# Performance work log

Measured on AMD Instinct MI355X. Metric: run time of the kernel, lower is better.

Reference implementation:

```python
import jax, jax.numpy as jnp
import numpy as np

D = 1024  # in_features
H = 16    # head_num

def setup_inputs() -> dict:
    key = jax.random.key(0)
    ks = jax.random.split(key, 11)
    S, B = 2048, 2
    scale = 1.0 / np.sqrt(D)
    inp = {
        'q': jax.random.normal(ks[0], (S, B, D), jnp.float32),
        'k': jax.random.normal(ks[1], (S, B, D), jnp.float32),
        'v': jax.random.normal(ks[2], (S, B, D), jnp.float32),
        'Wq': jax.random.normal(ks[3], (D, D), jnp.float32) * scale,
        'Wk': jax.random.normal(ks[4], (D, D), jnp.float32) * scale,
        'Wv': jax.random.normal(ks[5], (D, D), jnp.float32) * scale,
        'Wo': jax.random.normal(ks[6], (D, D), jnp.float32) * scale,
        'bq': jax.random.normal(ks[7], (D,), jnp.float32) * 0.01,
        'bk': jax.random.normal(ks[8], (D,), jnp.float32) * 0.01,
        'bv': jax.random.normal(ks[9], (D,), jnp.float32) * 0.01,
        'bo': jax.random.normal(ks[10], (D,), jnp.float32) * 0.01,
    }
    return inp

def reference(q, k, v, Wq, Wk, Wv, Wo, bq, bk, bv, bo):
    # q,k,v: (S, B, D) -> (B, S, D)
    q = jnp.transpose(q, (1, 0, 2))
    k = jnp.transpose(k, (1, 0, 2))
    v = jnp.transpose(v, (1, 0, 2))
    # linear + ReLU (torch Linear: x @ W.T + b)
    qh = jax.nn.relu(q @ Wq.T + bq)
    kh = jax.nn.relu(k @ Wk.T + bk)
    vh = jax.nn.relu(v @ Wv.T + bv)
    B, S, _ = qh.shape
    hd = D // H
    # (B, S, H, hd) -> (B, H, S, hd)
    qh = qh.reshape(B, S, H, hd).transpose(0, 2, 1, 3)
    kh = kh.reshape(B, S, H, hd).transpose(0, 2, 1, 3)
    vh = vh.reshape(B, S, H, hd).transpose(0, 2, 1, 3)
    scores = jnp.einsum('bhsd,bhtd->bhst', qh, kh) / np.sqrt(hd).astype(np.float32)
    attn = jax.nn.softmax(scores, axis=-1)
    y = jnp.einsum('bhst,bhtd->bhsd', attn, vh)  # (B, H, S, hd)
    y = y.transpose(0, 2, 1, 3).reshape(B, S, D)
    y = jax.nn.relu(y @ Wo.T + bo)
    return jnp.transpose(y, (1, 0, 2))  # (S, B, D)
```

## Files before the change

### kernel.cpp

```cpp
#include <hip/hip_runtime.h>
#include <stdint.h>

typedef __attribute__((ext_vector_type(8))) short bf8v;
typedef __attribute__((ext_vector_type(4))) float f4v;
typedef __attribute__((ext_vector_type(16))) float f16v;
typedef __attribute__((ext_vector_type(4))) unsigned int u4v;

__device__ __forceinline__ unsigned short f2bf(float f) {
  unsigned int u = __float_as_uint(f);
  u += 0x7fffu + ((u >> 16) & 1u);
  return (unsigned short)(u >> 16);
}

__device__ __forceinline__ void gload16(const void* g, void* l) {
  __builtin_amdgcn_global_load_lds(
      (__attribute__((address_space(1))) void*)reinterpret_cast<uintptr_t>(g),
      (__attribute__((address_space(3))) void*)reinterpret_cast<uintptr_t>(l),
      16, 0, 0);
}

__device__ __forceinline__ unsigned cvtpk(float lo, float hi) {
  unsigned r;
  asm("v_cvt_pk_bf16_f32 %0, %1, %2" : "=v"(r) : "v"(lo), "v"(hi));
  return r;
}

__global__ __launch_bounds__(256) void cvt_many(
    const float* __restrict__ s0, const float* __restrict__ s1,
    const float* __restrict__ s2, const float* __restrict__ s3,
    unsigned short* __restrict__ d0, unsigned short* __restrict__ d1,
    unsigned short* __restrict__ d2, unsigned short* __restrict__ d3, int n) {
  int a = blockIdx.y;
  const float* src = (a == 0) ? s0 : (a == 1) ? s1 : (a == 2) ? s2 : s3;
  unsigned short* dst = (a == 0) ? d0 : (a == 1) ? d1 : (a == 2) ? d2 : d3;
  int i = (blockIdx.x * 256 + threadIdx.x) * 8;
  if (i >= n) return;
  const f4v* sp = (const f4v*)(src + i);
  f4v x = sp[0], y = sp[1];
  bf8v r;
  r[0] = (short)f2bf(x[0]); r[1] = (short)f2bf(x[1]);
  r[2] = (short)f2bf(x[2]); r[3] = (short)f2bf(x[3]);
  r[4] = (short)f2bf(y[0]); r[5] = (short)f2bf(y[1]);
  r[6] = (short)f2bf(y[2]); r[7] = (short)f2bf(y[3]);
  *(bf8v*)(dst + i) = r;
}

template <int OMODE>
__device__ __forceinline__ void gemm_body(
    unsigned short* Al, unsigned short* Bl,
    const unsigned short* __restrict__ A, const unsigned short* __restrict__ W,
    const float* __restrict__ bias, void* __restrict__ out) {
  const int tid = threadIdx.x;
  const int w = tid >> 6, l = tid & 63;
  const int lr = l >> 4, lc = l & 15;
  const int m0 = blockIdx.x * 128, n0 = blockIdx.y * 128;
  const int wr = w >> 1, wc = w & 1;

  f4v acc[4][4];
#pragma unroll
  for (int i = 0; i < 4; i++)
#pragma unroll
    for (int j = 0; j < 4; j++) acc[i][j] = (f4v)(0.0f);

  const int NK = 32;
#pragma unroll
  for (int i = 0; i < 2; i++) {
    int chunk = w * 2 + i;
    int e = (chunk * 1024 + l * 16) >> 1;
    int r = e >> 5, k = e & 31;
    gload16(A + (size_t)(m0 + r) * 1024 + k, Al + chunk * 512);
    gload16(W + (size_t)(n0 + r) * 1024 + k, Bl + chunk * 512);
  }

  for (int kk = 0; kk < NK; kk++) {
    const int cur = kk & 1;
    __syncthreads();
    if (kk + 1 < NK) {
#pragma unroll
      for (int i = 0; i < 2; i++) {
        int chunk = w * 2 + i;
        int e = (chunk * 1024 + l * 16) >> 1;
        int r = e >> 5, k = (kk + 1) * 32 + (e & 31);
        gload16(A + (size_t)(m0 + r) * 1024 + k, Al + (cur ^ 1) * 4096 + chunk * 512);
        gload16(W + (size_t)(n0 + r) * 1024 + k, Bl + (cur ^ 1) * 4096 + chunk * 512);
      }
    }
    bf8v av[4], bv[4];
#pragma unroll
    for (int i = 0; i < 4; i++) {
      int row = wr * 64 + i * 16 + lc;
      av[i] = *(const bf8v*)(Al + cur * 4096 + row * 32 + lr * 8);
    }
#pragma unroll
    for (int j = 0; j < 4; j++) {
      int row = wc * 64 + j * 16 + lc;
      bv[j] = *(const bf8v*)(Bl + cur * 4096 + row * 32 + lr * 8);
    }
#pragma unroll
    for (int i = 0; i < 4; i++)
#pragma unroll
      for (int j = 0; j < 4; j++)
        acc[i][j] = __builtin_amdgcn_mfma_f32_16x16x32_bf16(av[i], bv[j], acc[i][j], 0, 0, 0);
  }

#pragma unroll
  for (int j = 0; j < 4; j++) {
    int n = n0 + wc * 64 + j * 16 + lc;
    float bj = bias[n];
#pragma unroll
    for (int i = 0; i < 4; i++) {
      int mb = m0 + wr * 64 + i * 16 + lr * 4;
#pragma unroll
      for (int q = 0; q < 4; q++) {
        float val = fmaxf(acc[i][j][q] + bj, 0.0f);
        int m = mb + q;
        if (OMODE == 2) {
          int s = m & 2047, b = m >> 11;
          ((float*)out)[(size_t)(s * 2 + b) * 1024 + n] = val;
        } else {
          int s = m >> 1, b = m & 1;
          int h = n >> 6, d = n & 63;
          if (OMODE == 0)
            ((unsigned short*)out)[((size_t)(b * 16 + h) * 2048 + s) * 64 + d] = f2bf(val);
          else
            ((unsigned short*)out)[((size_t)(b * 16 + h) * 64 + d) * 2048 + s] = f2bf(val);
        }
      }
    }
  }
}

__global__ __launch_bounds__(256) void qkv_gemm(
    const unsigned short* __restrict__ qA, const unsigned short* __restrict__ kA,
    const unsigned short* __restrict__ vA,
    const unsigned short* __restrict__ Wq, const unsigned short* __restrict__ Wk,
    const unsigned short* __restrict__ Wv,
    const float* __restrict__ bq, const float* __restrict__ bk,
    const float* __restrict__ bv,
    unsigned short* __restrict__ Qh, unsigned short* __restrict__ Kh,
    unsigned short* __restrict__ Vt) {
  __shared__ __align__(16) unsigned short Al[2 * 4096];
  __shared__ __align__(16) unsigned short Bl[2 * 4096];
  int z = blockIdx.z;
  if (z == 0)      gemm_body<0>(Al, Bl, qA, Wq, bq, Qh);
  else if (z == 1) gemm_body<0>(Al, Bl, kA, Wk, bk, Kh);
  else             gemm_body<1>(Al, Bl, vA, Wv, bv, Vt);
}

__global__ __launch_bounds__(256) void out_gemm(
    const unsigned short* __restrict__ Y, const unsigned short* __restrict__ Wo,
    const float* __restrict__ bo, float* __restrict__ out) {
  __shared__ __align__(16) unsigned short Al[2 * 4096];
  __shared__ __align__(16) unsigned short Bl[2 * 4096];
  gemm_body<2>(Al, Bl, Y, Wo, bo, out);
}

__global__ __launch_bounds__(128, 1) void attn_kernel(
    const unsigned short* __restrict__ Qh, const unsigned short* __restrict__ Kh,
    const unsigned short* __restrict__ Vt, unsigned short* __restrict__ Y) {
  __shared__ __align__(16) unsigned short Kl[2][4096];
  __shared__ __align__(16) unsigned short Vl[2][4096];
  const int tid = threadIdx.x, w = tid >> 6, l = tid & 63;
  const int lo = l & 31, hi = l >> 5;
  const int bh = blockIdx.y;
  const int q0 = blockIdx.x * 128 + w * 64;
  const size_t qkbase = (size_t)bh * 2048 * 64;
  const size_t vtbase = (size_t)bh * 64 * 2048;
  const float cs = 0.125f * 1.44269504088896341f;

  bf8v qf[2][4];
#pragma unroll
  for (int s = 0; s < 2; s++)
#pragma unroll
    for (int c = 0; c < 4; c++)
      qf[s][c] = *(const bf8v*)(Qh + qkbase + (size_t)(q0 + s * 32 + lo) * 64 + c * 16 + hi * 8);

  f16v oacc[2][2];
#pragma unroll
  for (int s = 0; s < 2; s++)
#pragma unroll
    for (int dt = 0; dt < 2; dt++) oacc[s][dt] = (f16v)(0.0f);
  float mrun[2] = {-1e30f, -1e30f}, lrun[2] = {0.0f, 0.0f};

  const int swl = (lo & 7) << 4;
  int akb[4], avb[2][2][2];
#pragma unroll
  for (int c = 0; c < 4; c++) akb[c] = lo * 128 + ((c * 32 + hi * 16) ^ swl);
#pragma unroll
  for (int dt = 0; dt < 2; dt++)
#pragma unroll
    for (int kvh = 0; kvh < 2; kvh++)
#pragma unroll
      for (int kc = 0; kc < 2; kc++)
        avb[dt][kvh][kc] = (dt * 32 + lo) * 128 + ((kvh * 64 + kc * 32 + hi * 16) ^ swl);

  int stE[4], stD[4], stKV[4];
#pragma unroll
  for (int i = 0; i < 4; i++) {
    int o = (w * 4 + i) * 1024 + l * 16;
    int row = o >> 7;
    stE[i] = (o ^ ((row & 7) << 4)) >> 1;
    stD[i] = stE[i] >> 6;
    stKV[i] = stE[i] & 63;
  }
  const char* KlB = (const char*)&Kl[0][0];
  const char* VlB = (const char*)&Vl[0][0];

  auto STAGE = [&](int buf, int t0) {
#pragma unroll
    for (int i = 0; i < 4; i++) {
      gload16(Kh + qkbase + (size_t)t0 * 64 + stE[i], (char*)&Kl[buf][0] + (w * 4 + i) * 1024);
      gload16(Vt + vtbase + (size_t)stD[i] * 2048 + t0 + stKV[i], (char*)&Vl[buf][0] + (w * 4 + i) * 1024);
    }
  };

  auto COMPUTE = [&](int bo) {
#pragma unroll
    for (int kvh = 0; kvh < 2; kvh++) {
      bf8v kf[4];
#pragma unroll
      for (int c = 0; c < 4; c++)
        kf[c] = *(const bf8v*)(KlB + bo + kvh * 4096 + akb[c]);
      f16v sa = (f16v)(0.0f), sb = (f16v)(0.0f);
#pragma unroll
      for (int c = 0; c < 4; c++) {
        sa = __builtin_amdgcn_mfma_f32_32x32x16_bf16(kf[c], qf[0][c], sa, 0, 0, 0);
        sb = __builtin_amdgcn_mfma_f32_32x32x16_bf16(kf[c], qf[1][c], sb, 0, 0, 0);
      }
      bf8v vf[2][2];
#pragma unroll
      for (int dt = 0; dt < 2; dt++)
#pragma unroll
        for (int kc = 0; kc < 2; kc++)
          vf[dt][kc] = *(const bf8v*)(VlB + bo + avb[dt][kvh][kc]);

#pragma unroll
      for (int s = 0; s < 2; s++) {
        const f16v& sc16 = (s == 0) ? sa : sb;
        float m16 = sc16[0];
#pragma unroll
        for (int r = 1; r < 16; r++) m16 = fmaxf(m16, sc16[r]);
        m16 = fmaxf(m16, __shfl_xor(m16, 32));
        float msc = m16 * cs;
        if (!__all(msc <= mrun[s] + 8.0f)) {
          float mnew = fmaxf(mrun[s], msc);
          float scl = __builtin_amdgcn_exp2f(mrun[s] - mnew);
          lrun[s] *= scl;
#pragma unroll
          for (int dt = 0; dt < 2; dt++)
#pragma unroll
            for (int r = 0; r < 16; r++) oacc[s][dt][r] *= scl;
          mrun[s] = mnew;
        }
        float p[16];
        float rs = 0.0f;
#pragma unroll
        for (int r = 0; r < 16; r++) {
          p[r] = __builtin_amdgcn_exp2f(sc16[r] * cs - mrun[s]);
          rs += p[r];
        }
        rs += __shfl_xor(rs, 32);
        lrun[s] += rs;
        bf8v pf[2];
#pragma unroll
        for (int kc = 0; kc < 2; kc++) {
          unsigned a0 = cvtpk(p[kc * 8 + 0], p[kc * 8 + 1]);
          unsigned a1 = cvtpk(p[kc * 8 + 2], p[kc * 8 + 3]);
          unsigned b0 = cvtpk(p[kc * 8 + 4], p[kc * 8 + 5]);
          unsigned b1 = cvtpk(p[kc * 8 + 6], p[kc * 8 + 7]);
          asm("v_permlane32_swap_b32 %0, %1" : "+v"(a0), "+v"(b0));
          asm("v_permlane32_swap_b32 %0, %1" : "+v"(a1), "+v"(b1));
          u4v pw;
          pw[0] = a0; pw[1] = a1; pw[2] = b0; pw[3] = b1;
          pf[kc] = __builtin_bit_cast(bf8v, pw);
        }
#pragma unroll
        for (int dt = 0; dt < 2; dt++)
#pragma unroll
          for (int kc = 0; kc < 2; kc++)
            oacc[s][dt] = __builtin_amdgcn_mfma_f32_32x32x16_bf16(vf[dt][kc], pf[kc], oacc[s][dt], 0, 0, 0);
      }
    }
  };

  STAGE(0, 0);
  __syncthreads();
#pragma unroll 1
  for (int t0 = 0; t0 < 2048; t0 += 128) {
    STAGE(1, t0 + 64);
    COMPUTE(0);
    __syncthreads();
    if (t0 + 128 < 2048) STAGE(0, t0 + 128);
    COMPUTE(8192);
    __syncthreads();
  }

  const int b = bh >> 4, h = bh & 15;
#pragma unroll
  for (int s = 0; s < 2; s++) {
    float inv = 1.0f / lrun[s];
    int q = q0 + s * 32 + lo;
    size_t base = ((size_t)(b * 2048 + q) << 10) + h * 64;
#pragma unroll
    for (int dt = 0; dt < 2; dt++)
#pragma unroll
      for (int r = 0; r < 16; r++) {
        int d = dt * 32 + (r & 3) + 8 * (r >> 2) + 4 * hi;
        Y[base + d] = f2bf(oacc[s][dt][r] * inv);
      }
  }
}

extern "C" void kernel_launch(void* const* d_in, const int* in_sizes, int n_in,
                              void* d_out, int out_size, void* d_ws, size_t ws_size,
                              hipStream_t stream) {
  const float* q  = (const float*)d_in[0];
  const float* k  = (const float*)d_in[1];
  const float* v  = (const float*)d_in[2];
  const float* Wq = (const float*)d_in[3];
  const float* Wk = (const float*)d_in[4];
  const float* Wv = (const float*)d_in[5];
  const float* Wo = (const float*)d_in[6];
  const float* bq = (const float*)d_in[7];
  const float* bk = (const float*)d_in[8];
  const float* bv = (const float*)d_in[9];
  const float* bo = (const float*)d_in[10];

  const size_t NA = (size_t)4096 * 1024;
  const size_t NW = (size_t)1024 * 1024;
  unsigned short* qA  = (unsigned short*)d_ws;
  unsigned short* kA  = qA  + NA;
  unsigned short* vA  = kA  + NA;
  unsigned short* WqB = vA  + NA;
  unsigned short* WkB = WqB + NW;
  unsigned short* WvB = WkB + NW;
  unsigned short* WoB = WvB + NW;
  unsigned short* Qh  = WoB + NW;
  unsigned short* Kh  = Qh  + NA;
  unsigned short* Vt  = Kh  + NA;
  unsigned short* Y   = Vt  + NA;

  cvt_many<<<dim3(2048, 3), 256, 0, stream>>>(q, k, v, nullptr, qA, kA, vA, nullptr, (int)NA);
  cvt_many<<<dim3(512, 4), 256, 0, stream>>>(Wq, Wk, Wv, Wo, WqB, WkB, WvB, WoB, (int)NW);

  qkv_gemm<<<dim3(32, 8, 3), 256, 0, stream>>>(qA, kA, vA, WqB, WkB, WvB,
                                               bq, bk, bv, Qh, Kh, Vt);
  attn_kernel<<<dim3(16, 32), 128, 0, stream>>>(Qh, Kh, Vt, Y);
  out_gemm<<<dim3(32, 8), 256, 0, stream>>>(Y, WoB, bo, (float*)d_out);
}
```

Measured before the change: 137.3 us.

## Load K/V directly to registers in attention and merge conversion launches

The attention kernel drops its LDS double-buffered staging with global_load_lds and barriers. Each single-wave block now loads K and V fragments straight from global memory into registers, ping-ponging between two register sets with 32-key steps, and the grid doubles to 32x32 blocks of 64 threads. The two fp32-to-bf16 conversion launches become one flat launch over the contiguous workspace, and the max reduction is rebalanced into a tree. This removes LDS traffic, syncs and one launch, at the cost of K/V reuse across waves, uncoalesced strided V loads, and more register pressure.

```diff
diff --git a/kernel.cpp b/kernel.cpp
--- a/kernel.cpp
+++ b/kernel.cpp
@@ -25,17 +25,26 @@
   return r;
 }
 
-__global__ __launch_bounds__(256) void cvt_many(
+__global__ __launch_bounds__(256) void cvt_all(
     const float* __restrict__ s0, const float* __restrict__ s1,
     const float* __restrict__ s2, const float* __restrict__ s3,
-    unsigned short* __restrict__ d0, unsigned short* __restrict__ d1,
-    unsigned short* __restrict__ d2, unsigned short* __restrict__ d3, int n) {
-  int a = blockIdx.y;
-  const float* src = (a == 0) ? s0 : (a == 1) ? s1 : (a == 2) ? s2 : s3;
-  unsigned short* dst = (a == 0) ? d0 : (a == 1) ? d1 : (a == 2) ? d2 : d3;
-  int i = (blockIdx.x * 256 + threadIdx.x) * 8;
-  if (i >= n) return;
-  const f4v* sp = (const f4v*)(src + i);
+    const float* __restrict__ s4, const float* __restrict__ s5,
+    const float* __restrict__ s6, unsigned short* __restrict__ dst) {
+  const size_t NA = (size_t)1 << 22, NW = (size_t)1 << 20;
+  size_t i = ((size_t)blockIdx.x * 256 + threadIdx.x) * 8;
+  const float* src;
+  size_t off;
+  if (i < 3 * NA) {
+    int a = (int)(i >> 22);
+    src = (a == 0) ? s0 : (a == 1) ? s1 : s2;
+    off = i & (NA - 1);
+  } else {
+    size_t j = i - 3 * NA;
+    int a = (int)(j >> 20);
+    src = (a == 0) ? s3 : (a == 1) ? s4 : (a == 2) ? s5 : s6;
+    off = j & (NW - 1);
+  }
+  const f4v* sp = (const f4v*)(src + off);
   f4v x = sp[0], y = sp[1];
   bf8v r;
   r[0] = (short)f2bf(x[0]); r[1] = (short)f2bf(x[1]);
@@ -155,17 +164,15 @@
   gemm_body<2>(Al, Bl, Y, Wo, bo, out);
 }
 
-__global__ __launch_bounds__(128, 1) void attn_kernel(
+__global__ __launch_bounds__(64, 1) void attn_kernel(
     const unsigned short* __restrict__ Qh, const unsigned short* __restrict__ Kh,
     const unsigned short* __restrict__ Vt, unsigned short* __restrict__ Y) {
-  __shared__ __align__(16) unsigned short Kl[2][4096];
-  __shared__ __align__(16) unsigned short Vl[2][4096];
-  const int tid = threadIdx.x, w = tid >> 6, l = tid & 63;
+  const int l = threadIdx.x & 63;
   const int lo = l & 31, hi = l >> 5;
   const int bh = blockIdx.y;
-  const int q0 = blockIdx.x * 128 + w * 64;
-  const size_t qkbase = (size_t)bh * 2048 * 64;
-  const size_t vtbase = (size_t)bh * 64 * 2048;
+  const int q0 = blockIdx.x * 64;
+  const unsigned short* __restrict__ Kb = Kh + (size_t)bh * 2048 * 64;
+  const unsigned short* __restrict__ Vb = Vt + (size_t)bh * 64 * 2048;
   const float cs = 0.125f * 1.44269504088896341f;
 
   bf8v qf[2][4];
@@ -173,7 +180,8 @@
   for (int s = 0; s < 2; s++)
 #pragma unroll
     for (int c = 0; c < 4; c++)
-      qf[s][c] = *(const bf8v*)(Qh + qkbase + (size_t)(q0 + s * 32 + lo) * 64 + c * 16 + hi * 8);
+      qf[s][c] = *(const bf8v*)(Qh + (size_t)bh * 2048 * 64 +
+                                (size_t)(q0 + s * 32 + lo) * 64 + c * 16 + hi * 8);
 
   f16v oacc[2][2];
 #pragma unroll
@@ -182,117 +190,85 @@
     for (int dt = 0; dt < 2; dt++) oacc[s][dt] = (f16v)(0.0f);
   float mrun[2] = {-1e30f, -1e30f}, lrun[2] = {0.0f, 0.0f};
 
-  const int swl = (lo & 7) << 4;
-  int akb[4], avb[2][2][2];
-#pragma unroll
-  for (int c = 0; c < 4; c++) akb[c] = lo * 128 + ((c * 32 + hi * 16) ^ swl);
-#pragma unroll
-  for (int dt = 0; dt < 2; dt++)
-#pragma unroll
-    for (int kvh = 0; kvh < 2; kvh++)
+  auto LOADKV = [&](bf8v (&kf)[4], bf8v (&vf)[4], int t) {
+#pragma unroll
+    for (int c = 0; c < 4; c++)
+      kf[c] = *(const bf8v*)(Kb + (size_t)(t + lo) * 64 + c * 16 + hi * 8);
+#pragma unroll
+    for (int dt = 0; dt < 2; dt++)
 #pragma unroll
       for (int kc = 0; kc < 2; kc++)
-        avb[dt][kvh][kc] = (dt * 32 + lo) * 128 + ((kvh * 64 + kc * 32 + hi * 16) ^ swl);
-
-  int stE[4], stD[4], stKV[4];
-#pragma unroll
-  for (int i = 0; i < 4; i++) {
-    int o = (w * 4 + i) * 1024 + l * 16;
-    int row = o >> 7;
-    stE[i] = (o ^ ((row & 7) << 4)) >> 1;
-    stD[i] = stE[i] >> 6;
-    stKV[i] = stE[i] & 63;
-  }
-  const char* KlB = (const char*)&Kl[0][0];
-  const char* VlB = (const char*)&Vl[0][0];
-
-  auto STAGE = [&](int buf, int t0) {
-#pragma unroll
-    for (int i = 0; i < 4; i++) {
-      gload16(Kh + qkbase + (size_t)t0 * 64 + stE[i], (char*)&Kl[buf][0] + (w * 4 + i) * 1024);
-      gload16(Vt + vtbase + (size_t)stD[i] * 2048 + t0 + stKV[i], (char*)&Vl[buf][0] + (w * 4 + i) * 1024);
-    }
+        vf[dt * 2 + kc] = *(const bf8v*)(Vb + (size_t)(dt * 32 + lo) * 2048 +
+                                         t + kc * 16 + hi * 8);
   };
 
-  auto COMPUTE = [&](int bo) {
-#pragma unroll
-    for (int kvh = 0; kvh < 2; kvh++) {
-      bf8v kf[4];
-#pragma unroll
-      for (int c = 0; c < 4; c++)
-        kf[c] = *(const bf8v*)(KlB + bo + kvh * 4096 + akb[c]);
-      f16v sa = (f16v)(0.0f), sb = (f16v)(0.0f);
-#pragma unroll
-      for (int c = 0; c < 4; c++) {
-        sa = __builtin_amdgcn_mfma_f32_32x32x16_bf16(kf[c], qf[0][c], sa, 0, 0, 0);
-        sb = __builtin_amdgcn_mfma_f32_32x32x16_bf16(kf[c], qf[1][c], sb, 0, 0, 0);
-      }
-      bf8v vf[2][2];
+  auto COMPUTE = [&](const bf8v (&kf)[4], const bf8v (&vf)[4]) {
+    f16v sa = (f16v)(0.0f), sb = (f16v)(0.0f);
+#pragma unroll
+    for (int c = 0; c < 4; c++) {
+      sa = __builtin_amdgcn_mfma_f32_32x32x16_bf16(kf[c], qf[0][c], sa, 0, 0, 0);
+      sb = __builtin_amdgcn_mfma_f32_32x32x16_bf16(kf[c], qf[1][c], sb, 0, 0, 0);
+    }
+#pragma unroll
+    for (int s = 0; s < 2; s++) {
+      const f16v& sc16 = (s == 0) ? sa : sb;
+      float m0a = fmaxf(fmaxf(sc16[0], sc16[1]), sc16[2]);
+      float m0b = fmaxf(fmaxf(sc16[3], sc16[4]), sc16[5]);
+      float m0c = fmaxf(fmaxf(sc16[6], sc16[7]), sc16[8]);
+      float m0d = fmaxf(fmaxf(sc16[9], sc16[10]), sc16[11]);
+      float m0e = fmaxf(fmaxf(sc16[12], sc16[13]), sc16[14]);
+      float m16 = fmaxf(fmaxf(fmaxf(m0a, m0b), fmaxf(m0c, m0d)), fmaxf(m0e, sc16[15]));
+      m16 = fmaxf(m16, __shfl_xor(m16, 32));
+      float msc = m16 * cs;
+      if (!__all(msc <= mrun[s] + 8.0f)) {
+        float mnew = fmaxf(mrun[s], msc);
+        float scl = __builtin_amdgcn_exp2f(mrun[s] - mnew);
+        lrun[s] *= scl;
+#pragma unroll
+        for (int dt = 0; dt < 2; dt++)
+#pragma unroll
+          for (int r = 0; r < 16; r++) oacc[s][dt][r] *= scl;
+        mrun[s] = mnew;
+      }
+      float p[16];
+      float rs = 0.0f;
+#pragma unroll
+      for (int r = 0; r < 16; r++) {
+        p[r] = __builtin_amdgcn_exp2f(sc16[r] * cs - mrun[s]);
+        rs += p[r];
+      }
+      rs += __shfl_xor(rs, 32);
+      lrun[s] += rs;
+      bf8v pf[2];
+#pragma unroll
+      for (int kc = 0; kc < 2; kc++) {
+        unsigned a0 = cvtpk(p[kc * 8 + 0], p[kc * 8 + 1]);
+        unsigned a1 = cvtpk(p[kc * 8 + 2], p[kc * 8 + 3]);
+        unsigned b0 = cvtpk(p[kc * 8 + 4], p[kc * 8 + 5]);
+        unsigned b1 = cvtpk(p[kc * 8 + 6], p[kc * 8 + 7]);
+        asm("v_permlane32_swap_b32 %0, %1" : "+v"(a0), "+v"(b0));
+        asm("v_permlane32_swap_b32 %0, %1" : "+v"(a1), "+v"(b1));
+        u4v pw;
+        pw[0] = a0; pw[1] = a1; pw[2] = b0; pw[3] = b1;
+        pf[kc] = __builtin_bit_cast(bf8v, pw);
+      }
 #pragma unroll
       for (int dt = 0; dt < 2; dt++)
 #pragma unroll
         for (int kc = 0; kc < 2; kc++)
-          vf[dt][kc] = *(const bf8v*)(VlB + bo + avb[dt][kvh][kc]);
-
-#pragma unroll
-      for (int s = 0; s < 2; s++) {
-        const f16v& sc16 = (s == 0) ? sa : sb;
-        float m16 = sc16[0];
-#pragma unroll
-        for (int r = 1; r < 16; r++) m16 = fmaxf(m16, sc16[r]);
-        m16 = fmaxf(m16, __shfl_xor(m16, 32));
-        float msc = m16 * cs;
-        if (!__all(msc <= mrun[s] + 8.0f)) {
-          float mnew = fmaxf(mrun[s], msc);
-          float scl = __builtin_amdgcn_exp2f(mrun[s] - mnew);
-          lrun[s] *= scl;
-#pragma unroll
-          for (int dt = 0; dt < 2; dt++)
-#pragma unroll
-            for (int r = 0; r < 16; r++) oacc[s][dt][r] *= scl;
-          mrun[s] = mnew;
-        }
-        float p[16];
-        float rs = 0.0f;
-#pragma unroll
-        for (int r = 0; r < 16; r++) {
-          p[r] = __builtin_amdgcn_exp2f(sc16[r] * cs - mrun[s]);
-          rs += p[r];
-        }
-        rs += __shfl_xor(rs, 32);
-        lrun[s] += rs;
-        bf8v pf[2];
-#pragma unroll
-        for (int kc = 0; kc < 2; kc++) {
-          unsigned a0 = cvtpk(p[kc * 8 + 0], p[kc * 8 + 1]);
-          unsigned a1 = cvtpk(p[kc * 8 + 2], p[kc * 8 + 3]);
-          unsigned b0 = cvtpk(p[kc * 8 + 4], p[kc * 8 + 5]);
-          unsigned b1 = cvtpk(p[kc * 8 + 6], p[kc * 8 + 7]);
-          asm("v_permlane32_swap_b32 %0, %1" : "+v"(a0), "+v"(b0));
-          asm("v_permlane32_swap_b32 %0, %1" : "+v"(a1), "+v"(b1));
-          u4v pw;
-          pw[0] = a0; pw[1] = a1; pw[2] = b0; pw[3] = b1;
-          pf[kc] = __builtin_bit_cast(bf8v, pw);
-        }
-#pragma unroll
-        for (int dt = 0; dt < 2; dt++)
-#pragma unroll
-          for (int kc = 0; kc < 2; kc++)
-            oacc[s][dt] = __builtin_amdgcn_mfma_f32_32x32x16_bf16(vf[dt][kc], pf[kc], oacc[s][dt], 0, 0, 0);
-      }
+          oacc[s][dt] = __builtin_amdgcn_mfma_f32_32x32x16_bf16(vf[dt * 2 + kc], pf[kc],
+                                                               oacc[s][dt], 0, 0, 0);
     }
   };
 
-  STAGE(0, 0);
-  __syncthreads();
+  bf8v kA[4], vA[4], kB[4], vB[4];
+  LOADKV(kA, vA, 0);
 #pragma unroll 1
-  for (int t0 = 0; t0 < 2048; t0 += 128) {
-    STAGE(1, t0 + 64);
-    COMPUTE(0);
-    __syncthreads();
-    if (t0 + 128 < 2048) STAGE(0, t0 + 128);
-    COMPUTE(8192);
-    __syncthreads();
+  for (int t = 0; t < 2048; t += 64) {
+    LOADKV(kB, vB, t + 32);
+    COMPUTE(kA, vA);
+    if (t + 64 < 2048) LOADKV(kA, vA, t + 64);
+    COMPUTE(kB, vB);
   }
 
   const int b = bh >> 4, h = bh & 15;
@@ -340,11 +316,10 @@
   unsigned short* Vt  = Kh  + NA;
   unsigned short* Y   = Vt  + NA;
 
-  cvt_many<<<dim3(2048, 3), 256, 0, stream>>>(q, k, v, nullptr, qA, kA, vA, nullptr, (int)NA);
-  cvt_many<<<dim3(512, 4), 256, 0, stream>>>(Wq, Wk, Wv, Wo, WqB, WkB, WvB, WoB, (int)NW);
+  cvt_all<<<dim3(8192), 256, 0, stream>>>(q, k, v, Wq, Wk, Wv, Wo, qA);
 
   qkv_gemm<<<dim3(32, 8, 3), 256, 0, stream>>>(qA, kA, vA, WqB, WkB, WvB,
                                                bq, bk, bv, Qh, Kh, Vt);
-  attn_kernel<<<dim3(16, 32), 128, 0, stream>>>(Qh, Kh, Vt, Y);
+  attn_kernel<<<dim3(32, 32), 64, 0, stream>>>(Qh, Kh, Vt, Y);
   out_gemm<<<dim3(32, 8), 256, 0, stream>>>(Y, WoB, bo, (float*)d_out);
 }
```

New measurement: 168.9 us. +23.0%, slower.

## Split attention query rows across four waves and merge conversion launches

Applied to the files above, without the earlier changes.

The attention kernel now runs 256 threads per block. Each wave handles 32 query rows instead of 64, and K/V staging is split over four waves. The aim is to raise occupancy and latency hiding, at the cost of less K/V fragment reuse per LDS read. The two fp32-to-bf16 conversion launches are merged into one flat kernel that writes into a contiguous workspace, removing one launch.

```diff
diff --git a/kernel.cpp b/kernel.cpp
--- a/kernel.cpp
+++ b/kernel.cpp
@@ -25,17 +25,26 @@
   return r;
 }
 
-__global__ __launch_bounds__(256) void cvt_many(
+__global__ __launch_bounds__(256) void cvt_all(
     const float* __restrict__ s0, const float* __restrict__ s1,
     const float* __restrict__ s2, const float* __restrict__ s3,
-    unsigned short* __restrict__ d0, unsigned short* __restrict__ d1,
-    unsigned short* __restrict__ d2, unsigned short* __restrict__ d3, int n) {
-  int a = blockIdx.y;
-  const float* src = (a == 0) ? s0 : (a == 1) ? s1 : (a == 2) ? s2 : s3;
-  unsigned short* dst = (a == 0) ? d0 : (a == 1) ? d1 : (a == 2) ? d2 : d3;
-  int i = (blockIdx.x * 256 + threadIdx.x) * 8;
-  if (i >= n) return;
-  const f4v* sp = (const f4v*)(src + i);
+    const float* __restrict__ s4, const float* __restrict__ s5,
+    const float* __restrict__ s6, unsigned short* __restrict__ dst) {
+  const size_t NA = (size_t)1 << 22, NW = (size_t)1 << 20;
+  size_t i = ((size_t)blockIdx.x * 256 + threadIdx.x) * 8;
+  const float* src;
+  size_t off;
+  if (i < 3 * NA) {
+    int a = (int)(i >> 22);
+    src = (a == 0) ? s0 : (a == 1) ? s1 : s2;
+    off = i & (NA - 1);
+  } else {
+    size_t j = i - 3 * NA;
+    int a = (int)(j >> 20);
+    src = (a == 0) ? s3 : (a == 1) ? s4 : (a == 2) ? s5 : s6;
+    off = j & (NW - 1);
+  }
+  const f4v* sp = (const f4v*)(src + off);
   f4v x = sp[0], y = sp[1];
   bf8v r;
   r[0] = (short)f2bf(x[0]); r[1] = (short)f2bf(x[1]);
@@ -155,7 +164,7 @@
   gemm_body<2>(Al, Bl, Y, Wo, bo, out);
 }
 
-__global__ __launch_bounds__(128, 1) void attn_kernel(
+__global__ __launch_bounds__(256, 2) void attn_kernel(
     const unsigned short* __restrict__ Qh, const unsigned short* __restrict__ Kh,
     const unsigned short* __restrict__ Vt, unsigned short* __restrict__ Y) {
   __shared__ __align__(16) unsigned short Kl[2][4096];
@@ -163,24 +172,20 @@
   const int tid = threadIdx.x, w = tid >> 6, l = tid & 63;
   const int lo = l & 31, hi = l >> 5;
   const int bh = blockIdx.y;
-  const int q0 = blockIdx.x * 128 + w * 64;
+  const int q0 = blockIdx.x * 128 + w * 32;
   const size_t qkbase = (size_t)bh * 2048 * 64;
   const size_t vtbase = (size_t)bh * 64 * 2048;
   const float cs = 0.125f * 1.44269504088896341f;
 
-  bf8v qf[2][4];
-#pragma unroll
-  for (int s = 0; s < 2; s++)
-#pragma unroll
-    for (int c = 0; c < 4; c++)
-      qf[s][c] = *(const bf8v*)(Qh + qkbase + (size_t)(q0 + s * 32 + lo) * 64 + c * 16 + hi * 8);
-
-  f16v oacc[2][2];
-#pragma unroll
-  for (int s = 0; s < 2; s++)
-#pragma unroll
-    for (int dt = 0; dt < 2; dt++) oacc[s][dt] = (f16v)(0.0f);
-  float mrun[2] = {-1e30f, -1e30f}, lrun[2] = {0.0f, 0.0f};
+  bf8v qf[4];
+#pragma unroll
+  for (int c = 0; c < 4; c++)
+    qf[c] = *(const bf8v*)(Qh + qkbase + (size_t)(q0 + lo) * 64 + c * 16 + hi * 8);
+
+  f16v oacc[2];
+  oacc[0] = (f16v)(0.0f);
+  oacc[1] = (f16v)(0.0f);
+  float mrun = -1e30f, lrun = 0.0f;
 
   const int swl = (lo & 7) << 4;
   int akb[4], avb[2][2][2];
@@ -194,10 +199,10 @@
       for (int kc = 0; kc < 2; kc++)
         avb[dt][kvh][kc] = (dt * 32 + lo) * 128 + ((kvh * 64 + kc * 32 + hi * 16) ^ swl);
 
-  int stE[4], stD[4], stKV[4];
-#pragma unroll
-  for (int i = 0; i < 4; i++) {
-    int o = (w * 4 + i) * 1024 + l * 16;
+  int stE[2], stD[2], stKV[2];
+#pragma unroll
+  for (int i = 0; i < 2; i++) {
+    int o = (w * 2 + i) * 1024 + l * 16;
     int row = o >> 7;
     stE[i] = (o ^ ((row & 7) << 4)) >> 1;
     stD[i] = stE[i] >> 6;
@@ -208,9 +213,9 @@
 
   auto STAGE = [&](int buf, int t0) {
 #pragma unroll
-    for (int i = 0; i < 4; i++) {
-      gload16(Kh + qkbase + (size_t)t0 * 64 + stE[i], (char*)&Kl[buf][0] + (w * 4 + i) * 1024);
-      gload16(Vt + vtbase + (size_t)stD[i] * 2048 + t0 + stKV[i], (char*)&Vl[buf][0] + (w * 4 + i) * 1024);
+    for (int i = 0; i < 2; i++) {
+      gload16(Kh + qkbase + (size_t)t0 * 64 + stE[i], (char*)&Kl[buf][0] + (w * 2 + i) * 1024);
+      gload16(Vt + vtbase + (size_t)stD[i] * 2048 + t0 + stKV[i], (char*)&Vl[buf][0] + (w * 2 + i) * 1024);
     }
   };
 
@@ -221,12 +226,10 @@
 #pragma unroll
       for (int c = 0; c < 4; c++)
         kf[c] = *(const bf8v*)(KlB + bo + kvh * 4096 + akb[c]);
-      f16v sa = (f16v)(0.0f), sb = (f16v)(0.0f);
-#pragma unroll
-      for (int c = 0; c < 4; c++) {
-        sa = __builtin_amdgcn_mfma_f32_32x32x16_bf16(kf[c], qf[0][c], sa, 0, 0, 0);
-        sb = __builtin_amdgcn_mfma_f32_32x32x16_bf16(kf[c], qf[1][c], sb, 0, 0, 0);
-      }
+      f16v sc16 = (f16v)(0.0f);
+#pragma unroll
+      for (int c = 0; c < 4; c++)
+        sc16 = __builtin_amdgcn_mfma_f32_32x32x16_bf16(kf[c], qf[c], sc16, 0, 0, 0);
       bf8v vf[2][2];
 #pragma unroll
       for (int dt = 0; dt < 2; dt++)
@@ -234,52 +237,51 @@
         for (int kc = 0; kc < 2; kc++)
           vf[dt][kc] = *(const bf8v*)(VlB + bo + avb[dt][kvh][kc]);
 
-#pragma unroll
-      for (int s = 0; s < 2; s++) {
-        const f16v& sc16 = (s == 0) ? sa : sb;
-        float m16 = sc16[0];
-#pragma unroll
-        for (int r = 1; r < 16; r++) m16 = fmaxf(m16, sc16[r]);
-        m16 = fmaxf(m16, __shfl_xor(m16, 32));
-        float msc = m16 * cs;
-        if (!__all(msc <= mrun[s] + 8.0f)) {
-          float mnew = fmaxf(mrun[s], msc);
-          float scl = __builtin_amdgcn_exp2f(mrun[s] - mnew);
-          lrun[s] *= scl;
-#pragma unroll
-          for (int dt = 0; dt < 2; dt++)
-#pragma unroll
-            for (int r = 0; r < 16; r++) oacc[s][dt][r] *= scl;
-          mrun[s] = mnew;
-        }
-        float p[16];
-        float rs = 0.0f;
-#pragma unroll
-        for (int r = 0; r < 16; r++) {
-          p[r] = __builtin_amdgcn_exp2f(sc16[r] * cs - mrun[s]);
-          rs += p[r];
-        }
-        rs += __shfl_xor(rs, 32);
-        lrun[s] += rs;
-        bf8v pf[2];
-#pragma unroll
-        for (int kc = 0; kc < 2; kc++) {
-          unsigned a0 = cvtpk(p[kc * 8 + 0], p[kc * 8 + 1]);
-          unsigned a1 = cvtpk(p[kc * 8 + 2], p[kc * 8 + 3]);
-          unsigned b0 = cvtpk(p[kc * 8 + 4], p[kc * 8 + 5]);
-          unsigned b1 = cvtpk(p[kc * 8 + 6], p[kc * 8 + 7]);
-          asm("v_permlane32_swap_b32 %0, %1" : "+v"(a0), "+v"(b0));
-          asm("v_permlane32_swap_b32 %0, %1" : "+v"(a1), "+v"(b1));
-          u4v pw;
-          pw[0] = a0; pw[1] = a1; pw[2] = b0; pw[3] = b1;
-          pf[kc] = __builtin_bit_cast(bf8v, pw);
-        }
+      float m0a = fmaxf(fmaxf(sc16[0], sc16[1]), sc16[2]);
+      float m0b = fmaxf(fmaxf(sc16[3], sc16[4]), sc16[5]);
+      float m0c = fmaxf(fmaxf(sc16[6], sc16[7]), sc16[8]);
+      float m0d = fmaxf(fmaxf(sc16[9], sc16[10]), sc16[11]);
+      float m0e = fmaxf(fmaxf(sc16[12], sc16[13]), sc16[14]);
+      float m16 = fmaxf(fmaxf(fmaxf(m0a, m0b), fmaxf(m0c, m0d)), fmaxf(m0e, sc16[15]));
+      m16 = fmaxf(m16, __shfl_xor(m16, 32));
+      float msc = m16 * cs;
+      if (!__all(msc <= mrun + 8.0f)) {
+        float mnew = fmaxf(mrun, msc);
+        float scl = __builtin_amdgcn_exp2f(mrun - mnew);
+        lrun *= scl;
 #pragma unroll
         for (int dt = 0; dt < 2; dt++)
 #pragma unroll
-          for (int kc = 0; kc < 2; kc++)
-            oacc[s][dt] = __builtin_amdgcn_mfma_f32_32x32x16_bf16(vf[dt][kc], pf[kc], oacc[s][dt], 0, 0, 0);
-      }
+          for (int r = 0; r < 16; r++) oacc[dt][r] *= scl;
+        mrun = mnew;
+      }
+      float p[16];
+      float rs = 0.0f;
+#pragma unroll
+      for (int r = 0; r < 16; r++) {
+        p[r] = __builtin_amdgcn_exp2f(sc16[r] * cs - mrun);
+        rs += p[r];
+      }
+      rs += __shfl_xor(rs, 32);
+      lrun += rs;
+      bf8v pf[2];
+#pragma unroll
+      for (int kc = 0; kc < 2; kc++) {
+        unsigned a0 = cvtpk(p[kc * 8 + 0], p[kc * 8 + 1]);
+        unsigned a1 = cvtpk(p[kc * 8 + 2], p[kc * 8 + 3]);
+        unsigned b0 = cvtpk(p[kc * 8 + 4], p[kc * 8 + 5]);
+        unsigned b1 = cvtpk(p[kc * 8 + 6], p[kc * 8 + 7]);
+        asm("v_permlane32_swap_b32 %0, %1" : "+v"(a0), "+v"(b0));
+        asm("v_permlane32_swap_b32 %0, %1" : "+v"(a1), "+v"(b1));
+        u4v pw;
+        pw[0] = a0; pw[1] = a1; pw[2] = b0; pw[3] = b1;
+        pf[kc] = __builtin_bit_cast(bf8v, pw);
+      }
+#pragma unroll
+      for (int dt = 0; dt < 2; dt++)
+#pragma unroll
+        for (int kc = 0; kc < 2; kc++)
+          oacc[dt] = __builtin_amdgcn_mfma_f32_32x32x16_bf16(vf[dt][kc], pf[kc], oacc[dt], 0, 0, 0);
     }
   };
 
@@ -296,17 +298,16 @@
   }
 
   const int b = bh >> 4, h = bh & 15;
-#pragma unroll
-  for (int s = 0; s < 2; s++) {
-    float inv = 1.0f / lrun[s];
-    int q = q0 + s * 32 + lo;
+  {
+    float inv = 1.0f / lrun;
+    int q = q0 + lo;
     size_t base = ((size_t)(b * 2048 + q) << 10) + h * 64;
 #pragma unroll
     for (int dt = 0; dt < 2; dt++)
 #pragma unroll
       for (int r = 0; r < 16; r++) {
         int d = dt * 32 + (r & 3) + 8 * (r >> 2) + 4 * hi;
-        Y[base + d] = f2bf(oacc[s][dt][r] * inv);
+        Y[base + d] = f2bf(oacc[dt][r] * inv);
       }
   }
 }
@@ -340,11 +341,10 @@
   unsigned short* Vt  = Kh  + NA;
   unsigned short* Y   = Vt  + NA;
 
-  cvt_many<<<dim3(2048, 3), 256, 0, stream>>>(q, k, v, nullptr, qA, kA, vA, nullptr, (int)NA);
-  cvt_many<<<dim3(512, 4), 256, 0, stream>>>(Wq, Wk, Wv, Wo, WqB, WkB, WvB, WoB, (int)NW);
+  cvt_all<<<dim3(8192), 256, 0, stream>>>(q, k, v, Wq, Wk, Wv, Wo, qA);
 
   qkv_gemm<<<dim3(32, 8, 3), 256, 0, stream>>>(qA, kA, vA, WqB, WkB, WvB,
                                                bq, bk, bv, Qh, Kh, Vt);
-  attn_kernel<<<dim3(16, 32), 128, 0, stream>>>(Qh, Kh, Vt, Y);
+  attn_kernel<<<dim3(16, 32), 256, 0, stream>>>(Qh, Kh, Vt, Y);
   out_gemm<<<dim3(32, 8), 256, 0, stream>>>(Y, WoB, bo, (float*)d_out);
 }
```

After: 128.5 us. 6.4% less time.
